# Kernel tuning notes

Hardware: AMD Instinct MI355X
Metric: run time of the kernel (lower is better)

Reference implementation:

```python
import jax, jax.numpy as jnp
from jax import lax
import numpy as np

B, D_IN, L, D, K, DS = 8, 16, 4096, 512, 4, 4
BLOCKS = (1, 2, 3, 4)          # block sizes, all offset 0 (max_block_size=4)
PAD_MULT = 12                  # lcm(1,2,3,4)


def setup_inputs() -> dict:
    key = jax.random.key(0)
    ks = jax.random.split(key, 5)
    return {
        "x": jax.random.normal(ks[0], (B, D_IN, L), jnp.float32),
        "conv_w": jax.random.normal(ks[1], (D, D_IN, K), jnp.float32) * 0.05,
        "conv_b": jax.random.normal(ks[2], (D,), jnp.float32) * 0.02,
        "score_w": jax.random.normal(ks[3], (D,), jnp.float32) * 0.02,
        "score_b": jax.random.normal(ks[4], (1,), jnp.float32) * 0.02,
    }


def reference(x, conv_w, conv_b, score_w, score_b):
    # pos_conv: Conv1d(padding='same', k=4). Torch 'same' with even kernel pads
    # left=(k-1)//2=1, right=2.
    h = lax.conv_general_dilated(x, conv_w, (1,), [(1, 2)],
                                 dimension_numbers=('NCH', 'OIH', 'NCH'))
    h = jnp.transpose(h, (0, 2, 1)) + conv_b            # [B, L, D]

    Np = -(-L // PAD_MULT) * PAD_MULT                   # pad seq to multiple of 12
    h = jnp.pad(h, ((0, 0), (0, Np - L), (0, 0)))       # [B, Np, D]

    # per-block-size mean pooling, then broadcast back to char resolution
    reprs = []
    for m in BLOCKS:
        r = h.reshape(B, Np // m, m, D).mean(axis=2)    # [B, Np/m, D]
        reprs.append(jnp.repeat(r, m, axis=1))          # [B, Np, D]
    br = jnp.stack(reprs, axis=2)                       # [B, Np, nb, D]

    # score each block representation, softmax over block sizes
    scores = jnp.einsum('bnmd,d->bnm', br, score_w) + score_b[0]
    scores = jax.nn.softmax(scores, axis=2)             # [B, Np, nb]

    # consensus attention across positions over the nb-dim score vectors
    sim = jnp.einsum('bim,bjm->bij', scores, scores)    # [B, Np, Np]
    attn = jax.nn.softmax(sim, axis=-1)
    scores = jnp.einsum('bij,bjm->bim', attn, scores)   # [B, Np, nb]

    # weighted sum of block reprs
    xo = jnp.einsum('bnmd,bnm->bnd', br, scores)        # [B, Np, D]

    mlen = -(-L // DS) * DS                              # 4096 (== L here)
    char_x = xo[:, :mlen]
    xd = char_x.reshape(B, mlen // DS, DS, D).mean(axis=2)  # [B, L/DS, D]
    return char_x[:, :L], xd
```

## Files before the change

kernel.cpp:

```cpp
#include <hip/hip_runtime.h>
#include <hip/hip_bf16.h>

#define B_ 8
#define DIN 16
#define L_ 4096
#define D_ 512
#define NP 4104
#define NG 342
#define JSP 32
#define JCH 129

__device__ __forceinline__ unsigned short f2bf(float f) {
  unsigned int u = __float_as_uint(f);
  unsigned int r = (u + 0x7fffu + ((u >> 16) & 1u)) >> 16;
  return (unsigned short)r;
}
__device__ __forceinline__ float bf2f(unsigned int u) {
  return __uint_as_float(u << 16);
}

__device__ __constant__ float D5[6] = {0.9999544f, 1.0005163f, 0.4975827f,
                                       0.1726558f, 0.0334570f, 0.0140872f};
__device__ __constant__ float FACT[6] = {1.f, 1.f, 2.f, 6.f, 24.f, 120.f};

__global__ __launch_bounds__(256) void k_conv(
    const float* __restrict__ x, const float* __restrict__ cw,
    const float* __restrict__ cb, unsigned short* __restrict__ h) {
  __shared__ float ws_w[64 * 132];
  __shared__ float ws_x[DIN * 40];
  int bid = blockIdx.x;
  int dtile = bid & 3;
  int ntile = (bid >> 2) & 127;
  int b = bid >> 9;
  int n0 = ntile * 32;
  int d0 = dtile * 128;
  int tid = threadIdx.x;

  for (int q = tid; q < 128 * 16; q += 256) {
    int dd = q >> 4, qq = (q & 15) << 2;
    float4 wv = *reinterpret_cast<const float4*>(cw + ((size_t)(d0 + dd) << 6) + qq);
    *reinterpret_cast<float4*>(&ws_w[(dd >> 1) * 132 + (dd & 1) * 64 + qq]) = wv;
  }
  const float* xb = x + (size_t)b * DIN * L_;
  for (int q = tid; q < DIN * 40; q += 256) {
    int i = q / 40, c = q - i * 40;
    int nx = n0 + c - 4;
    ws_x[q] = (nx >= 0 && nx < L_) ? xb[i * L_ + nx] : 0.0f;
  }
  __syncthreads();

  int dp = tid & 63;
  int seg = tid >> 6;
  float acc0[8], acc1[8];
#pragma unroll
  for (int j = 0; j < 8; ++j) { acc0[j] = 0.f; acc1[j] = 0.f; }

  for (int i = 0; i < DIN; ++i) {
    const float* wp = &ws_w[dp * 132 + (i << 2)];
    float w00 = wp[0], w01 = wp[1], w02 = wp[2], w03 = wp[3];
    float w10 = wp[64], w11 = wp[65], w12 = wp[66], w13 = wp[67];
    const float* xp = &ws_x[i * 40 + (seg << 3)];
    float xr[16];
#pragma unroll
    for (int m = 0; m < 16; ++m) xr[m] = xp[m];
#pragma unroll
    for (int j = 0; j < 8; ++j) {
      float a0 = acc0[j], a1 = acc1[j];
      a0 = fmaf(w00, xr[j + 3], a0);
      a0 = fmaf(w01, xr[j + 4], a0);
      a0 = fmaf(w02, xr[j + 5], a0);
      a0 = fmaf(w03, xr[j + 6], a0);
      a1 = fmaf(w10, xr[j + 3], a1);
      a1 = fmaf(w11, xr[j + 4], a1);
      a1 = fmaf(w12, xr[j + 5], a1);
      a1 = fmaf(w13, xr[j + 6], a1);
      acc0[j] = a0; acc1[j] = a1;
    }
  }
  int d = d0 + (dp << 1);
  float cb0 = cb[d], cb1 = cb[d + 1];
  unsigned short* hb = h + (size_t)b * L_ * D_;
#pragma unroll
  for (int j = 0; j < 8; ++j) {
    int n = n0 + (seg << 3) + j;
    unsigned int pv = (unsigned int)f2bf(acc0[j] + cb0) |
                      ((unsigned int)f2bf(acc1[j] + cb1) << 16);
    *reinterpret_cast<unsigned int*>(&hb[(size_t)n * D_ + d]) = pv;
  }
}

__global__ __launch_bounds__(256) void k_uprep(
    const float* __restrict__ cw, const float* __restrict__ cb,
    const float* __restrict__ sw, float* __restrict__ us) {
  __shared__ float red[4][64];
  __shared__ float red2[64];
  int t = threadIdx.x;
  int p = t & 63, chunk = t >> 6;
  float s = 0.f;
  for (int d = chunk * 128; d < chunk * 128 + 128; ++d)
    s = fmaf(sw[d], cw[((size_t)d << 6) + p], s);
  red[chunk][p] = s;
  if (t < 64) {
    float pc = 0.f;
    for (int j = 0; j < 8; ++j) pc = fmaf(sw[t + 64 * j], cb[t + 64 * j], pc);
    red2[t] = pc;
  }
  __syncthreads();
  if (t < 64) us[t] = red[0][t] + red[1][t] + red[2][t] + red[3][t];
  if (t == 0) {
    float c0 = 0.f;
    for (int j = 0; j < 64; ++j) c0 += red2[j];
    us[64] = c0;
  }
}

__global__ __launch_bounds__(192) void k_scores(
    const float* __restrict__ x, const float* __restrict__ us,
    const float* __restrict__ sb, unsigned short* __restrict__ s0) {
  __shared__ float xs[DIN * 195];
  __shared__ float ul[65];
  __shared__ float tb[192];
  int bid = blockIdx.x;
  int b = bid / 22, blk = bid - b * 22;
  int base0 = blk * 192;
  int t = threadIdx.x;
  const float* xb = x + (size_t)b * DIN * L_;
  for (int q = t; q < DIN * 195; q += 192) {
    int i = q / 195, c = q - i * 195;
    int nx = base0 - 1 + c;
    xs[q] = (nx >= 0 && nx < L_) ? xb[i * L_ + nx] : 0.f;
  }
  if (t < 65) ul[t] = us[t];
  __syncthreads();
  int n = base0 + t;
  float tv = 0.f;
  if (n < L_) {
    tv = ul[64];
    for (int i = 0; i < DIN; ++i) {
#pragma unroll
      for (int k = 0; k < 4; ++k)
        tv = fmaf(xs[i * 195 + t + k], ul[(i << 2) + k], tv);
    }
  }
  tb[t] = tv;
  __syncthreads();
  if (n < NP) {
    float t1 = tb[t];
    int e2 = t & ~1;
    float t2 = 0.5f * (tb[e2] + tb[e2 + 1]);
    int e3 = (t / 3) * 3;
    float t3 = (1.f / 3.f) * (tb[e3] + tb[e3 + 1] + tb[e3 + 2]);
    int e4 = t & ~3;
    float t4 = 0.25f * (tb[e4] + tb[e4 + 1] + tb[e4 + 2] + tb[e4 + 3]);
    float sbv = sb[0];
    float c0s = t1 + sbv, c1s = t2 + sbv, c2s = t3 + sbv, c3s = t4 + sbv;
    float mx = fmaxf(fmaxf(c0s, c1s), fmaxf(c2s, c3s));
    float e0 = __expf(c0s - mx), e1 = __expf(c1s - mx);
    float e2f = __expf(c2s - mx), e3f = __expf(c3s - mx);
    float inv = 1.f / (e0 + e1 + e2f + e3f);
    ushort4 ov;
    ov.x = f2bf(e0 * inv); ov.y = f2bf(e1 * inv);
    ov.z = f2bf(e2f * inv); ov.w = f2bf(e3f * inv);
    *reinterpret_cast<ushort4*>(&s0[(((size_t)b * NP) + n) << 2]) = ov;
  }
}

__global__ __launch_bounds__(256) void k_moment(
    const unsigned short* __restrict__ s0, float* __restrict__ Mpart) {
  __shared__ float sv[JCH][4];
  __shared__ float ls[JCH][4];
  __shared__ float mp[4][128][5];
  int bid = blockIdx.x;
  int js = bid & 31;
  int b = bid >> 5;
  int t = threadIdx.x;
  int lane = t & 63, wv = t >> 6;
  int jlo = js * JCH;
  int cnt = NP - jlo; if (cnt > JCH) cnt = JCH;

  const ushort4* sp = reinterpret_cast<const ushort4*>(s0) + (size_t)b * NP + jlo;
  for (int r = t; r < cnt; r += 256) {
    ushort4 u = sp[r];
    float v0 = bf2f(u.x), v1 = bf2f(u.y), v2 = bf2f(u.z), v3 = bf2f(u.w);
    sv[r][0] = v0; sv[r][1] = v1; sv[r][2] = v2; sv[r][3] = v3;
    ls[r][0] = __log2f(v0); ls[r][1] = __log2f(v1);
    ls[r][2] = __log2f(v2); ls[r][3] = __log2f(v3);
  }
  int f1 = lane, f2 = lane + 64;
  float e1a = 0.f, e1b = 0.f, e1c = 0.f, e1d = 0.f;
  float e2a = 0.f, e2b = 0.f, e2c = 0.f, e2d = 0.f;
  {
    int f = 0;
    for (int a = 0; a <= 5; ++a)
      for (int b2 = 0; b2 <= 5 - a; ++b2)
        for (int c = 0; c <= 5 - a - b2; ++c)
          for (int d2 = 0; d2 <= 5 - a - b2 - c; ++d2) {
            if (f == f1) { e1a = a; e1b = b2; e1c = c; e1d = d2; }
            if (f == f2) { e2a = a; e2b = b2; e2c = c; e2d = d2; }
            ++f;
          }
  }
  __syncthreads();
  float acc1[5] = {0.f, 0.f, 0.f, 0.f, 0.f};
  float acc2[5] = {0.f, 0.f, 0.f, 0.f, 0.f};
  for (int jj = wv; jj < cnt; jj += 4) {
    float4 lv = *reinterpret_cast<float4*>(&ls[jj][0]);
    float4 vv = *reinterpret_cast<float4*>(&sv[jj][0]);
    float t1 = e1a * lv.x;
    t1 = fmaf(e1b, lv.y, t1);
    t1 = fmaf(e1c, lv.z, t1);
    t1 = fmaf(e1d, lv.w, t1);
    float t2 = e2a * lv.x;
    t2 = fmaf(e2b, lv.y, t2);
    t2 = fmaf(e2c, lv.z, t2);
    t2 = fmaf(e2d, lv.w, t2);
    float m1 = exp2f(t1);
    float m2 = exp2f(t2);
    acc1[0] = fmaf(m1, vv.x, acc1[0]);
    acc1[1] = fmaf(m1, vv.y, acc1[1]);
    acc1[2] = fmaf(m1, vv.z, acc1[2]);
    acc1[3] = fmaf(m1, vv.w, acc1[3]);
    acc1[4] += m1;
    acc2[0] = fmaf(m2, vv.x, acc2[0]);
    acc2[1] = fmaf(m2, vv.y, acc2[1]);
    acc2[2] = fmaf(m2, vv.z, acc2[2]);
    acc2[3] = fmaf(m2, vv.w, acc2[3]);
    acc2[4] += m2;
  }
#pragma unroll
  for (int c = 0; c < 5; ++c) {
    mp[wv][lane][c] = acc1[c];
    mp[wv][lane + 64][c] = acc2[c];
  }
  __syncthreads();
  if (t < 630) {
    int f = t / 5, c = t - f * 5;
    float s = mp[0][f][c] + mp[1][f][c] + mp[2][f][c] + mp[3][f][c];
    Mpart[((size_t)(b * 32 + js)) * 640 + t] = s;
  }
}

__global__ __launch_bounds__(640) void k_mred(
    const float* __restrict__ Mpart, float* __restrict__ Mfin) {
  int b = blockIdx.x;
  int t = threadIdx.x;
  if (t >= 630) return;
  int f = t / 5, c = t - f * 5;
  float s = 0.f;
  for (int js = 0; js < JSP; ++js)
    s += Mpart[((size_t)(b * 32 + js)) * 640 + t];
  int fa = 0, fb = 0, fc = 0, fd = 0;
  {
    int ff = 0;
    for (int a = 0; a <= 5; ++a)
      for (int b2 = 0; b2 <= 5 - a; ++b2)
        for (int cc = 0; cc <= 5 - a - b2; ++cc)
          for (int d2 = 0; d2 <= 5 - a - b2 - cc; ++d2) {
            if (ff == f) { fa = a; fb = b2; fc = cc; fd = d2; }
            ++ff;
          }
  }
  int k = fa + fb + fc + fd;
  float w = D5[k] * FACT[k] / (FACT[fa] * FACT[fb] * FACT[fc] * FACT[fd]);
  Mfin[((size_t)b * 128 + f) * 8 + c] = w * s;
}

__global__ __launch_bounds__(256) void k_apply(
    const unsigned short* __restrict__ s0, const float* __restrict__ Mfin,
    float* __restrict__ s2) {
  __shared__ float M[128 * 8];
  int bid = blockIdx.x;
  int b = bid / 17, ch = bid - b * 17;
  int t = threadIdx.x;
  const float4* Mb = reinterpret_cast<const float4*>(Mfin + (size_t)b * 128 * 8);
  if (t < 252) *reinterpret_cast<float4*>(&M[t * 4]) = Mb[t];
  __syncthreads();
  int i = ch * 256 + t;
  if (i >= NP) return;
  ushort4 u = reinterpret_cast<const ushort4*>(s0)[(size_t)b * NP + i];
  float s_0 = bf2f(u.x), s_1 = bf2f(u.y), s_2 = bf2f(u.z), s_3 = bf2f(u.w);
  float a0 = 0.f, a1 = 0.f, a2 = 0.f, a3 = 0.f, az = 0.f;
  int f = 0;
  float pa = 1.f;
#pragma unroll
  for (int a = 0; a <= 5; ++a) {
    float pb = pa;
#pragma unroll
    for (int b2 = 0; b2 <= 5 - a; ++b2) {
      float pc = pb;
#pragma unroll
      for (int c = 0; c <= 5 - a - b2; ++c) {
        float run = pc;
#pragma unroll
        for (int d2 = 0; d2 <= 5 - a - b2 - c; ++d2) {
          const float* mf = &M[f * 8];
          float4 m4 = *reinterpret_cast<const float4*>(mf);
          a0 = fmaf(run, m4.x, a0);
          a1 = fmaf(run, m4.y, a1);
          a2 = fmaf(run, m4.z, a2);
          a3 = fmaf(run, m4.w, a3);
          az = fmaf(run, mf[4], az);
          run *= s_3;
          ++f;
        }
        pc *= s_2;
      }
      pb *= s_1;
    }
    pa *= s_0;
  }
  float inv = 1.f / az;
  reinterpret_cast<float4*>(s2)[(size_t)b * NP + i] =
      make_float4(a0 * inv, a1 * inv, a2 * inv, a3 * inv);
}

__global__ __launch_bounds__(256) void k_final(
    const unsigned short* __restrict__ h, const float* __restrict__ s2,
    float* __restrict__ out) {
  __shared__ float ss[12][4];
  int bid = blockIdx.x;
  int b = bid / NG, g = bid - b * NG;
  int base = g * 12;
  int t = threadIdx.x;
  if (t < 48) ((float*)ss)[t] = s2[((((size_t)b * NP) + base) << 2) + t];
  __syncthreads();
  int d = t << 1;
  const unsigned short* hb = h + (size_t)b * L_ * D_;
  float hv0[12], hv1[12];
#pragma unroll
  for (int j = 0; j < 12; ++j) {
    int n = base + j;
    if (n < L_) {
      unsigned int u = *reinterpret_cast<const unsigned int*>(&hb[(size_t)n * D_ + d]);
      hv0[j] = bf2f(u & 0xffffu); hv1[j] = bf2f(u >> 16);
    } else { hv0[j] = 0.f; hv1[j] = 0.f; }
  }
  float P20[6], P21[6], P30[4], P31[4], P40[3], P41[3];
#pragma unroll
  for (int q = 0; q < 6; ++q) {
    P20[q] = 0.5f * (hv0[2 * q] + hv0[2 * q + 1]);
    P21[q] = 0.5f * (hv1[2 * q] + hv1[2 * q + 1]);
  }
#pragma unroll
  for (int q = 0; q < 4; ++q) {
    P30[q] = (1.f / 3.f) * (hv0[3 * q] + hv0[3 * q + 1] + hv0[3 * q + 2]);
    P31[q] = (1.f / 3.f) * (hv1[3 * q] + hv1[3 * q + 1] + hv1[3 * q + 2]);
  }
#pragma unroll
  for (int q = 0; q < 3; ++q) {
    P40[q] = 0.25f * (hv0[4 * q] + hv0[4 * q + 1] + hv0[4 * q + 2] + hv0[4 * q + 3]);
    P41[q] = 0.25f * (hv1[4 * q] + hv1[4 * q + 1] + hv1[4 * q + 2] + hv1[4 * q + 3]);
  }
  float* outc = out;
  float* outd = out + (size_t)B_ * L_ * D_;
  float xq0[3] = {0.f, 0.f, 0.f}, xq1[3] = {0.f, 0.f, 0.f};
#pragma unroll
  for (int j = 0; j < 12; ++j) {
    float w0 = ss[j][0], w1 = ss[j][1], w2 = ss[j][2], w3 = ss[j][3];
    float v0 = w0 * hv0[j] + w1 * P20[j >> 1] + w2 * P30[j / 3] + w3 * P40[j >> 2];
    float v1 = w0 * hv1[j] + w1 * P21[j >> 1] + w2 * P31[j / 3] + w3 * P41[j >> 2];
    int n = base + j;
    if (n < L_) {
      float2 o; o.x = v0; o.y = v1;
      *reinterpret_cast<float2*>(&outc[((size_t)b * L_ + n) * D_ + d]) = o;
    }
    xq0[j >> 2] += v0; xq1[j >> 2] += v1;
  }
#pragma unroll
  for (int q = 0; q < 3; ++q) {
    int r = 3 * g + q;
    if (r < 1024) {
      float2 o; o.x = 0.25f * xq0[q]; o.y = 0.25f * xq1[q];
      *reinterpret_cast<float2*>(&outd[((size_t)b * 1024 + r) * D_ + d]) = o;
    }
  }
}

extern "C" void kernel_launch(void* const* d_in, const int* in_sizes, int n_in,
                              void* d_out, int out_size, void* d_ws, size_t ws_size,
                              hipStream_t stream) {
  const float* x = (const float*)d_in[0];
  const float* cw = (const float*)d_in[1];
  const float* cb = (const float*)d_in[2];
  const float* sw = (const float*)d_in[3];
  const float* sb = (const float*)d_in[4];
  float* out = (float*)d_out;
  char* ws = (char*)d_ws;
  unsigned short* h = (unsigned short*)ws;
  size_t off = 33554432;
  unsigned short* s0 = (unsigned short*)(ws + off);
  off += 262656;
  float* s2 = (float*)(ws + off);
  off += 525312;
  float* Mpart = (float*)(ws + off);
  off += 655360;
  float* Mfin = (float*)(ws + off);
  off += 32768;
  float* us = (float*)(ws + off);

  k_conv<<<4096, 256, 0, stream>>>(x, cw, cb, h);
  k_uprep<<<1, 256, 0, stream>>>(cw, cb, sw, us);
  k_scores<<<8 * 22, 192, 0, stream>>>(x, us, sb, s0);
  k_moment<<<B_ * JSP, 256, 0, stream>>>(s0, Mpart);
  k_mred<<<B_, 640, 0, stream>>>(Mpart, Mfin);
  k_apply<<<B_ * 17, 256, 0, stream>>>(s0, Mfin, s2);
  k_final<<<B_ * NG, 256, 0, stream>>>(h, s2, out);
}
```

Measured before the change: 92.44 us.

## Fuse positional conv into final weighted-sum kernel, dropping h intermediate

Removes the separate conv kernel and its bf16 h buffer; the final kernel now computes the conv for a 48-position span and 128 channels in registers and directly applies block pooling and score weighting. This eliminates the write and re-read of the intermediate activation tensor and one kernel launch. It also removes bf16 rounding of h, and idle segments past the padded length waste some compute.

```diff
diff --git a/kernel.cpp b/kernel.cpp
--- a/kernel.cpp
+++ b/kernel.cpp
@@ -9,6 +9,8 @@
 #define NG 342
 #define JSP 32
 #define JCH 129
+#define SPAN 48
+#define NSPAN 86
 
 __device__ __forceinline__ unsigned short f2bf(float f) {
   unsigned int u = __float_as_uint(f);
@@ -22,72 +24,6 @@
 __device__ __constant__ float D5[6] = {0.9999544f, 1.0005163f, 0.4975827f,
                                        0.1726558f, 0.0334570f, 0.0140872f};
 __device__ __constant__ float FACT[6] = {1.f, 1.f, 2.f, 6.f, 24.f, 120.f};
-
-__global__ __launch_bounds__(256) void k_conv(
-    const float* __restrict__ x, const float* __restrict__ cw,
-    const float* __restrict__ cb, unsigned short* __restrict__ h) {
-  __shared__ float ws_w[64 * 132];
-  __shared__ float ws_x[DIN * 40];
-  int bid = blockIdx.x;
-  int dtile = bid & 3;
-  int ntile = (bid >> 2) & 127;
-  int b = bid >> 9;
-  int n0 = ntile * 32;
-  int d0 = dtile * 128;
-  int tid = threadIdx.x;
-
-  for (int q = tid; q < 128 * 16; q += 256) {
-    int dd = q >> 4, qq = (q & 15) << 2;
-    float4 wv = *reinterpret_cast<const float4*>(cw + ((size_t)(d0 + dd) << 6) + qq);
-    *reinterpret_cast<float4*>(&ws_w[(dd >> 1) * 132 + (dd & 1) * 64 + qq]) = wv;
-  }
-  const float* xb = x + (size_t)b * DIN * L_;
-  for (int q = tid; q < DIN * 40; q += 256) {
-    int i = q / 40, c = q - i * 40;
-    int nx = n0 + c - 4;
-    ws_x[q] = (nx >= 0 && nx < L_) ? xb[i * L_ + nx] : 0.0f;
-  }
-  __syncthreads();
-
-  int dp = tid & 63;
-  int seg = tid >> 6;
-  float acc0[8], acc1[8];
-#pragma unroll
-  for (int j = 0; j < 8; ++j) { acc0[j] = 0.f; acc1[j] = 0.f; }
-
-  for (int i = 0; i < DIN; ++i) {
-    const float* wp = &ws_w[dp * 132 + (i << 2)];
-    float w00 = wp[0], w01 = wp[1], w02 = wp[2], w03 = wp[3];
-    float w10 = wp[64], w11 = wp[65], w12 = wp[66], w13 = wp[67];
-    const float* xp = &ws_x[i * 40 + (seg << 3)];
-    float xr[16];
-#pragma unroll
-    for (int m = 0; m < 16; ++m) xr[m] = xp[m];
-#pragma unroll
-    for (int j = 0; j < 8; ++j) {
-      float a0 = acc0[j], a1 = acc1[j];
-      a0 = fmaf(w00, xr[j + 3], a0);
-      a0 = fmaf(w01, xr[j + 4], a0);
-      a0 = fmaf(w02, xr[j + 5], a0);
-      a0 = fmaf(w03, xr[j + 6], a0);
-      a1 = fmaf(w10, xr[j + 3], a1);
-      a1 = fmaf(w11, xr[j + 4], a1);
-      a1 = fmaf(w12, xr[j + 5], a1);
-      a1 = fmaf(w13, xr[j + 6], a1);
-      acc0[j] = a0; acc1[j] = a1;
-    }
-  }
-  int d = d0 + (dp << 1);
-  float cb0 = cb[d], cb1 = cb[d + 1];
-  unsigned short* hb = h + (size_t)b * L_ * D_;
-#pragma unroll
-  for (int j = 0; j < 8; ++j) {
-    int n = n0 + (seg << 3) + j;
-    unsigned int pv = (unsigned int)f2bf(acc0[j] + cb0) |
-                      ((unsigned int)f2bf(acc1[j] + cb1) << 16);
-    *reinterpret_cast<unsigned int*>(&hb[(size_t)n * D_ + d]) = pv;
-  }
-}
 
 __global__ __launch_bounds__(256) void k_uprep(
     const float* __restrict__ cw, const float* __restrict__ cb,
@@ -314,26 +250,80 @@
       make_float4(a0 * inv, a1 * inv, a2 * inv, a3 * inv);
 }
 
-__global__ __launch_bounds__(256) void k_final(
-    const unsigned short* __restrict__ h, const float* __restrict__ s2,
+__global__ __launch_bounds__(256) void k_fused(
+    const float* __restrict__ x, const float* __restrict__ cw,
+    const float* __restrict__ cb, const float* __restrict__ s2,
     float* __restrict__ out) {
-  __shared__ float ss[12][4];
+  __shared__ float ws_w[64 * 132];
+  __shared__ float ws_x[DIN * 52];
+  __shared__ float ss[4][12][4];
   int bid = blockIdx.x;
-  int b = bid / NG, g = bid - b * NG;
+  int dtile = bid & 3;
+  int span = (bid >> 2) % NSPAN;
+  int b = bid / (4 * NSPAN);
+  int n0 = span * SPAN;
+  int d0 = dtile * 128;
+  int g0 = n0 / 12;
+  int tid = threadIdx.x;
+
+  for (int q = tid; q < 128 * 16; q += 256) {
+    int dd = q >> 4, qq = (q & 15) << 2;
+    float4 wv = *reinterpret_cast<const float4*>(cw + ((size_t)(d0 + dd) << 6) + qq);
+    *reinterpret_cast<float4*>(&ws_w[(dd >> 1) * 132 + (dd & 1) * 64 + qq]) = wv;
+  }
+  const float* xb = x + (size_t)b * DIN * L_;
+  for (int q = tid; q < DIN * 52; q += 256) {
+    int i = q / 52, c = q - i * 52;
+    int nx = n0 - 1 + c;
+    ws_x[q] = (c < 51 && nx >= 0 && nx < L_) ? xb[i * L_ + nx] : 0.f;
+  }
+  if (tid < 192) {
+    int gg = tid / 48, r = tid - gg * 48;
+    int g = g0 + gg;
+    ((float*)ss)[tid] = (g < NG) ? s2[((size_t)b * NP + g * 12) * 4 + r] : 0.f;
+  }
+  __syncthreads();
+
+  int dp = tid & 63;
+  int seg = tid >> 6;
+  int g = g0 + seg;
+  float acc0[12], acc1[12];
+#pragma unroll
+  for (int j = 0; j < 12; ++j) { acc0[j] = 0.f; acc1[j] = 0.f; }
+
+  for (int i = 0; i < DIN; ++i) {
+    const float* wp = &ws_w[dp * 132 + (i << 2)];
+    float w00 = wp[0], w01 = wp[1], w02 = wp[2], w03 = wp[3];
+    float w10 = wp[64], w11 = wp[65], w12 = wp[66], w13 = wp[67];
+    const float* xp = &ws_x[i * 52 + seg * 12];
+    float xr[16];
+#pragma unroll
+    for (int m = 0; m < 16; ++m) xr[m] = xp[m];
+#pragma unroll
+    for (int j = 0; j < 12; ++j) {
+      float a0 = acc0[j], a1 = acc1[j];
+      a0 = fmaf(w00, xr[j], a0);
+      a0 = fmaf(w01, xr[j + 1], a0);
+      a0 = fmaf(w02, xr[j + 2], a0);
+      a0 = fmaf(w03, xr[j + 3], a0);
+      a1 = fmaf(w10, xr[j], a1);
+      a1 = fmaf(w11, xr[j + 1], a1);
+      a1 = fmaf(w12, xr[j + 2], a1);
+      a1 = fmaf(w13, xr[j + 3], a1);
+      acc0[j] = a0; acc1[j] = a1;
+    }
+  }
+  if (g >= NG) return;
+
+  int d = d0 + (dp << 1);
+  float cb0 = cb[d], cb1 = cb[d + 1];
   int base = g * 12;
-  int t = threadIdx.x;
-  if (t < 48) ((float*)ss)[t] = s2[((((size_t)b * NP) + base) << 2) + t];
-  __syncthreads();
-  int d = t << 1;
-  const unsigned short* hb = h + (size_t)b * L_ * D_;
   float hv0[12], hv1[12];
 #pragma unroll
   for (int j = 0; j < 12; ++j) {
     int n = base + j;
-    if (n < L_) {
-      unsigned int u = *reinterpret_cast<const unsigned int*>(&hb[(size_t)n * D_ + d]);
-      hv0[j] = bf2f(u & 0xffffu); hv1[j] = bf2f(u >> 16);
-    } else { hv0[j] = 0.f; hv1[j] = 0.f; }
+    if (n < L_) { hv0[j] = acc0[j] + cb0; hv1[j] = acc1[j] + cb1; }
+    else { hv0[j] = 0.f; hv1[j] = 0.f; }
   }
   float P20[6], P21[6], P30[4], P31[4], P40[3], P41[3];
 #pragma unroll
@@ -356,7 +346,8 @@
   float xq0[3] = {0.f, 0.f, 0.f}, xq1[3] = {0.f, 0.f, 0.f};
 #pragma unroll
   for (int j = 0; j < 12; ++j) {
-    float w0 = ss[j][0], w1 = ss[j][1], w2 = ss[j][2], w3 = ss[j][3];
+    float w0 = ss[seg][j][0], w1 = ss[seg][j][1];
+    float w2 = ss[seg][j][2], w3 = ss[seg][j][3];
     float v0 = w0 * hv0[j] + w1 * P20[j >> 1] + w2 * P30[j / 3] + w3 * P40[j >> 2];
     float v1 = w0 * hv1[j] + w1 * P21[j >> 1] + w2 * P31[j / 3] + w3 * P41[j >> 2];
     int n = base + j;
@@ -386,8 +377,7 @@
   const float* sb = (const float*)d_in[4];
   float* out = (float*)d_out;
   char* ws = (char*)d_ws;
-  unsigned short* h = (unsigned short*)ws;
-  size_t off = 33554432;
+  size_t off = 0;
   unsigned short* s0 = (unsigned short*)(ws + off);
   off += 262656;
   float* s2 = (float*)(ws + off);
@@ -398,11 +388,10 @@
   off += 32768;
   float* us = (float*)(ws + off);
 
-  k_conv<<<4096, 256, 0, stream>>>(x, cw, cb, h);
   k_uprep<<<1, 256, 0, stream>>>(cw, cb, sw, us);
   k_scores<<<8 * 22, 192, 0, stream>>>(x, us, sb, s0);
   k_moment<<<B_ * JSP, 256, 0, stream>>>(s0, Mpart);
   k_mred<<<B_, 640, 0, stream>>>(Mpart, Mfin);
   k_apply<<<B_ * 17, 256, 0, stream>>>(s0, Mfin, s2);
-  k_final<<<B_ * NG, 256, 0, stream>>>(h, s2, out);
-}
+  k_fused<<<B_ * NSPAN * 4, 256, 0, stream>>>(x, cw, cb, s2, out);
+}
```

New measurement: 76.83 us. 1.2x faster.
